# Kernel optimization log

Measured on AMD Instinct MI355X. Metric: run time of the kernel, lower is better.

The kernel has to match this reference:

```python
import jax, jax.numpy as jnp
import numpy as np

N = 50000
E = 1600000
IN_DIM = 32
EDGE_DIM = 32
HID = 64
OUT = 32


def setup_inputs() -> dict:
    key = jax.random.key(0)
    ks = jax.random.split(key, 12)
    x = jax.random.normal(ks[0], (N, IN_DIM), dtype=jnp.float32)
    edge_index = jax.random.randint(ks[1], (2, E), 0, N, dtype=jnp.int64)
    edge_attr = jax.random.normal(ks[2], (E, EDGE_DIM), dtype=jnp.float32)
    # MLP params: Linear(64->64), Linear(64->128), Linear(128->64), Linear(64->32)
    def lin(k, fan_in, fan_out):
        lim = 1.0 / np.sqrt(fan_in)
        kw, kb = jax.random.split(k)
        W = jax.random.uniform(kw, (fan_in, fan_out), minval=-lim, maxval=lim, dtype=jnp.float32)
        b = jax.random.uniform(kb, (fan_out,), minval=-lim, maxval=lim, dtype=jnp.float32)
        return W, b
    W1, b1 = lin(ks[3], IN_DIM + EDGE_DIM, HID)
    W2, b2 = lin(ks[4], HID, 2 * HID)
    W3, b3 = lin(ks[5], 2 * HID, HID)
    W4, b4 = lin(ks[6], HID, OUT)
    return {"x": x, "edge_index": edge_index, "edge_attr": edge_attr,
            "W1": W1, "b1": b1, "W2": W2, "b2": b2,
            "W3": W3, "b3": b3, "W4": W4, "b4": b4}


def reference(x, edge_index, edge_attr, W1, b1, W2, b2, W3, b3, W4, b4):
    # PyG MessagePassing (source_to_target): x_i = x[edge_index[1]] (target),
    # messages aggregated (mean) at target nodes edge_index[1].
    dst = edge_index[1]
    x_i = x[dst]                                   # [E, IN_DIM] gather
    m = jnp.concatenate([x_i, edge_attr], axis=-1)  # [E, 64]
    # 4-layer MLP with ReLU (dropout = identity at inference)
    m = jax.nn.relu(m @ W1 + b1)                   # [E, 64]
    m = jax.nn.relu(m @ W2 + b2)                   # [E, 128]
    m = jax.nn.relu(m @ W3 + b3)                   # [E, 64]
    m = jax.nn.relu(m @ W4 + b4)                   # [E, 32]
    # mean scatter to target nodes
    sums = jax.ops.segment_sum(m, dst, num_segments=N)          # [N, 32]
    cnt = jax.ops.segment_sum(jnp.ones((E,), m.dtype), dst, num_segments=N)
    out = sums / jnp.maximum(cnt, 1.0)[:, None]
    return out
```

## Files before the change

kernel.cpp:

```cpp
#include <hip/hip_runtime.h>
#include <hip/hip_bf16.h>

typedef __attribute__((ext_vector_type(8))) unsigned short u16x8;
typedef __attribute__((ext_vector_type(8))) __bf16 bf16x8;
typedef __attribute__((ext_vector_type(4))) float f32x4;

__device__ __forceinline__ unsigned pack_bf2(float lo, float hi) {
  unsigned a = __float_as_uint(lo) + 0x8000u;
  unsigned b = __float_as_uint(hi) + 0x8000u;
  return __builtin_amdgcn_perm(b, a, 0x07060302);
}

__device__ __forceinline__ unsigned short f2bf(float f) {
  unsigned u = __float_as_uint(f);
  return (unsigned short)((u + 0x7fffu + ((u >> 16) & 1u)) >> 16);
}

__device__ __forceinline__ int aswz(int row, int feat, int stride) {
  return row * stride + (((feat >> 3) ^ (row & 7)) << 4) + (feat & 7) * 2;
}

__global__ void prep_weights(const float* __restrict__ W1, const float* __restrict__ W2,
                             const float* __restrict__ W3, const float* __restrict__ W4,
                             unsigned short* __restrict__ wt) {
  int i = blockIdx.x * 256 + threadIdx.x;
  if (i >= 22528) return;
  float v; int n, k, K, base;
  if (i < 4096)       { n = i >> 6, k = i & 63;  K = 64;  base = 0;     v = W1[k * 64 + n]; }
  else if (i < 12288) { int j = i - 4096;  n = j >> 6, k = j & 63;  K = 64;  base = 4096;  v = W2[k * 128 + n]; }
  else if (i < 20480) { int j = i - 12288; n = j >> 7, k = j & 127; K = 128; base = 12288; v = W3[k * 64 + n]; }
  else                { int j = i - 20480; n = j >> 6, k = j & 63;  K = 64;  base = 20480; v = W4[k * 32 + n]; }
  int o = base + n * K + ((((k >> 3) ^ (n & 7)) << 3) + (k & 7));
  wt[o] = f2bf(v);
}

__global__ void hist_kernel(const int* __restrict__ ei, int* __restrict__ histI, int E) {
  int e = blockIdx.x * 256 + threadIdx.x;
  if (e < E) atomicAdd(&histI[ei[E + e]], 1);
}

__global__ void scan_blocks(const int* __restrict__ histI, int* __restrict__ row_start,
                            int* __restrict__ blockSums, int N) {
  __shared__ int wsum[4];
  const int lane = threadIdx.x & 63, w = threadIdx.x >> 6;
  const int i0 = blockIdx.x * 2048 + threadIdx.x * 8;
  int v[8];
#pragma unroll
  for (int j = 0; j < 8; ++j) { int i = i0 + j; v[j] = (i < N) ? histI[i] : 0; }
  int s = 0;
#pragma unroll
  for (int j = 0; j < 8; ++j) { int t = v[j]; v[j] = s; s += t; }
  int ss = s;
#pragma unroll
  for (int d = 1; d < 64; d <<= 1) { int t = __shfl_up(ss, d, 64); if (lane >= d) ss += t; }
  if (lane == 63) wsum[w] = ss;
  __syncthreads();
  int wOff = 0;
#pragma unroll
  for (int k = 0; k < 4; ++k) if (k < w) wOff += wsum[k];
  const int tOff = wOff + (ss - s);
#pragma unroll
  for (int j = 0; j < 8; ++j) { int i = i0 + j; if (i < N) row_start[i] = tOff + v[j]; }
  if (threadIdx.x == 255) blockSums[blockIdx.x] = wOff + ss;
}

__global__ void scan_tops(int* __restrict__ blockSums, int nb) {
  const int lane = threadIdx.x;
  int v = (lane < nb) ? blockSums[lane] : 0;
  int s = v;
#pragma unroll
  for (int d = 1; d < 64; d <<= 1) { int t = __shfl_up(s, d, 64); if (lane >= d) s += t; }
  if (lane < nb) blockSums[lane] = s - v;
}

__global__ void scan_add(int* __restrict__ row_start, const int* __restrict__ blockSums, int N) {
  int i = blockIdx.x * 256 + threadIdx.x;
  if (i < N) row_start[i] += blockSums[i >> 11];
}

__global__ void fill_kernel(const int* __restrict__ ei, const int* __restrict__ row_start,
                            int* __restrict__ wcnt, int2* __restrict__ edlist, int E) {
  int e = blockIdx.x * 256 + threadIdx.x;
  if (e >= E) return;
  int d = ei[E + e];
  int slot = atomicAdd(&wcnt[d], 1);
  edlist[row_start[d] + slot] = make_int2(e, d);
}

template <int MT, int KS, int SS, int DS>
__device__ __forceinline__ void mlp_layer(const unsigned char* src, unsigned char* dst,
                                          const unsigned char* wl, const float* biasL, int lane) {
  const int edge = lane & 15, g = lane >> 4;
  asm volatile("s_waitcnt lgkmcnt(0)" ::: "memory");
  u16x8 bfrag[KS];
#pragma unroll
  for (int ks = 0; ks < KS; ++ks)
    bfrag[ks] = *(const u16x8*)(src + aswz(edge, ks * 32 + g * 8, SS));
#pragma unroll
  for (int mt = 0; mt < MT; ++mt) {
    const int n = mt * 16 + edge;
    u16x8 af[KS];
#pragma unroll
    for (int ks = 0; ks < KS; ++ks)
      af[ks] = *(const u16x8*)(wl + n * (KS * 64) + (((ks * 4 + g) ^ (edge & 7)) << 4));
    const float4 bv = *(const float4*)(biasL + mt * 16 + g * 4);
    f32x4 acc = {bv.x, bv.y, bv.z, bv.w};
    __builtin_amdgcn_s_setprio(1);
#pragma unroll
    for (int ks = 0; ks < KS; ++ks)
      acc = __builtin_amdgcn_mfma_f32_16x16x32_bf16(
          __builtin_bit_cast(bf16x8, af[ks]), __builtin_bit_cast(bf16x8, bfrag[ks]),
          acc, 0, 0, 0);
    __builtin_amdgcn_s_setprio(0);
    const int fb = mt * 16 + g * 4;
    uint2 q;
    q.x = pack_bf2(fmaxf(acc[0], 0.f), fmaxf(acc[1], 0.f));
    q.y = pack_bf2(fmaxf(acc[2], 0.f), fmaxf(acc[3], 0.f));
    *(uint2*)(dst + aswz(edge, fb, DS)) = q;
  }
}

__device__ __forceinline__ void load_tile(int ebase, int E, const int2* __restrict__ edlist,
                                          const float* __restrict__ x, const float* __restrict__ ea,
                                          int lane, float4& xa, float4& xb, float4& ya, float4& yb,
                                          int& dstA) {
  const int el = ebase + (lane >> 2);
  const int part = lane & 3;
  xa = make_float4(0.f, 0.f, 0.f, 0.f); xb = xa; ya = xa; yb = xa;
  if (el < E) {
    const int2 ed = edlist[el];
    const float4* xp = (const float4*)(x + (size_t)ed.y * 32 + part * 8);
    xa = xp[0]; xb = xp[1];
    const float4* ep = (const float4*)(ea + (size_t)ed.x * 32 + part * 8);
    ya = ep[0]; yb = ep[1];
  }
  const int pos = ebase + (lane & 15);
  dstA = (pos < E) ? edlist[pos].y : -1;
}

#define BIAS_OFF   45056
#define ACT_OFF    46208

__global__ __launch_bounds__(1024, 4)
void gnn_main(const float* __restrict__ x, const int2* __restrict__ edlist,
              const float* __restrict__ ea, const unsigned short* __restrict__ wt,
              const float* __restrict__ b1, const float* __restrict__ b2,
              const float* __restrict__ b3, const float* __restrict__ b4,
              float* __restrict__ out, int E, int numTiles) {
  __shared__ __align__(16) unsigned char lds[ACT_OFF + 16 * 6144];
  {
    const u16x8* gw = (const u16x8*)wt;
    u16x8* lw = (u16x8*)lds;
    for (int i = threadIdx.x; i < 2816; i += 1024) lw[i] = gw[i];
    float* biasW = (float*)(lds + BIAS_OFF);
    for (int i = threadIdx.x; i < 288; i += 1024) {
      float v;
      if (i < 64) v = b1[i];
      else if (i < 192) v = b2[i - 64];
      else if (i < 256) v = b3[i - 192];
      else v = b4[i - 256];
      biasW[i] = v;
    }
  }
  __syncthreads();

  const int lane = threadIdx.x & 63, wid = threadIdx.x >> 6;
  const int edge = lane & 15, g = lane >> 4;
  const float* biasLds = (const float*)(lds + BIAS_OFF);
  unsigned char* buf0 = lds + ACT_OFF + wid * 6144;
  unsigned char* buf1 = buf0 + 4096;
  const unsigned char* wl1 = lds;
  const unsigned char* wl2 = lds + 8192;
  const unsigned char* wl3 = lds + 24576;
  const unsigned char* wl4 = lds + 40960;

  const int wgl = blockIdx.x * 16 + wid;
  const int wstride = gridDim.x * 16;

  float4 xa, xb, ya, yb; int dstA = -1;
  if (wgl < numTiles) load_tile(wgl * 16, E, edlist, x, ea, lane, xa, xb, ya, yb, dstA);

  for (int tile = wgl; tile < numTiles; tile += wstride) {
    uint4 hx, he;
    hx.x = pack_bf2(xa.x, xa.y); hx.y = pack_bf2(xa.z, xa.w);
    hx.z = pack_bf2(xb.x, xb.y); hx.w = pack_bf2(xb.z, xb.w);
    he.x = pack_bf2(ya.x, ya.y); he.y = pack_bf2(ya.z, ya.w);
    he.z = pack_bf2(yb.x, yb.y); he.w = pack_bf2(yb.z, yb.w);
    const int e2 = lane >> 2, part = lane & 3;
    *(uint4*)(buf0 + aswz(e2, part * 8, 256)) = hx;
    *(uint4*)(buf0 + aswz(e2, 32 + part * 8, 256)) = he;

    const int curDst = dstA;

    const int nt = tile + wstride;
    float4 nxa, nxb, nya, nyb; int ndst = -1;
    if (nt < numTiles) load_tile(nt * 16, E, edlist, x, ea, lane, nxa, nxb, nya, nyb, ndst);
    else { nxa = make_float4(0,0,0,0); nxb = nxa; nya = nxa; nyb = nxa; }

    mlp_layer<4, 2, 256, 128>(buf0, buf1, wl1, biasLds + 0,   lane);
    mlp_layer<8, 2, 128, 256>(buf1, buf0, wl2, biasLds + 64,  lane);
    mlp_layer<4, 4, 256, 128>(buf0, buf1, wl3, biasLds + 192, lane);

    asm volatile("s_waitcnt lgkmcnt(0)" ::: "memory");
    u16x8 bf4[2];
#pragma unroll
    for (int ks = 0; ks < 2; ++ks)
      bf4[ks] = *(const u16x8*)(buf1 + aswz(edge, ks * 32 + g * 8, 128));
    float vals[8];
#pragma unroll
    for (int mt = 0; mt < 2; ++mt) {
      const int n = mt * 16 + edge;
      u16x8 af[2];
#pragma unroll
      for (int ks = 0; ks < 2; ++ks)
        af[ks] = *(const u16x8*)(wl4 + n * 128 + (((ks * 4 + g) ^ (edge & 7)) << 4));
      const float4 bv = *(const float4*)(biasLds + 256 + mt * 16 + g * 4);
      f32x4 acc = {bv.x, bv.y, bv.z, bv.w};
      __builtin_amdgcn_s_setprio(1);
#pragma unroll
      for (int ks = 0; ks < 2; ++ks)
        acc = __builtin_amdgcn_mfma_f32_16x16x32_bf16(
            __builtin_bit_cast(bf16x8, af[ks]), __builtin_bit_cast(bf16x8, bf4[ks]),
            acc, 0, 0, 0);
      __builtin_amdgcn_s_setprio(0);
#pragma unroll
      for (int r = 0; r < 4; ++r) vals[mt * 4 + r] = fmaxf(acc[r], 0.f);
    }

    const int li = edge;
    const int prev = __shfl_up(curDst, 1, 16);
    const bool is_head = (li == 0) || (prev != curDst);
    const unsigned long long hb = __ballot(is_head);
    const unsigned gm = (unsigned)((hb >> (g * 16)) & 0xFFFFu);
    const unsigned below = gm & ((1u << li) | ((1u << li) - 1u));
    const int dist = li - (31 - __clz(below));
#pragma unroll
    for (int d = 1; d < 16; d <<= 1) {
#pragma unroll
      for (int t = 0; t < 8; ++t) {
        const float tv = __shfl_up(vals[t], d, 16);
        if (dist >= d) vals[t] += tv;
      }
    }
    const bool is_end = (li == 15) || ((gm >> (li + 1)) & 1u);
    if (is_end && curDst >= 0) {
      float* op = out + (size_t)curDst * 32 + g * 4;
#pragma unroll
      for (int t = 0; t < 4; ++t) unsafeAtomicAdd(op + t, vals[t]);
#pragma unroll
      for (int t = 0; t < 4; ++t) unsafeAtomicAdd(op + 16 + t, vals[4 + t]);
    }

    xa = nxa; xb = nxb; ya = nya; yb = nyb; dstA = ndst;
  }
}

__global__ void div_kernel(float* __restrict__ out, const int* __restrict__ histI, int total) {
  int i = blockIdx.x * 256 + threadIdx.x;
  if (i < total) out[i] = out[i] / fmaxf((float)histI[i >> 5], 1.0f);
}

extern "C" void kernel_launch(void* const* d_in, const int* in_sizes, int n_in,
                              void* d_out, int out_size, void* d_ws, size_t ws_size,
                              hipStream_t stream) {
  const float* x  = (const float*)d_in[0];
  const int*   ei = (const int*)d_in[1];
  const float* ea = (const float*)d_in[2];
  const float* W1 = (const float*)d_in[3];
  const float* b1 = (const float*)d_in[4];
  const float* W2 = (const float*)d_in[5];
  const float* b2 = (const float*)d_in[6];
  const float* W3 = (const float*)d_in[7];
  const float* b3 = (const float*)d_in[8];
  const float* W4 = (const float*)d_in[9];
  const float* b4 = (const float*)d_in[10];
  const int N = in_sizes[0] / 32;
  const int E = in_sizes[1] / 2;
  float* out = (float*)d_out;

  char* ws = (char*)d_ws;
  size_t off = 0;
  auto alloc = [&](size_t bytes) { size_t o = off; off += (bytes + 255) & ~(size_t)255; return o; };
  int* histI      = (int*)(ws + alloc((size_t)N * 4));
  int* wcnt       = (int*)(ws + alloc((size_t)N * 4));
  int* row_start  = (int*)(ws + alloc((size_t)(N + 1) * 4));
  int* blockSums  = (int*)(ws + alloc(64 * 4));
  int2* edlist    = (int2*)(ws + alloc((size_t)E * 8));
  unsigned short* wt = (unsigned short*)(ws + alloc(22528 * 2));

  hipMemsetAsync(d_out, 0, (size_t)out_size * sizeof(float), stream);
  hipMemsetAsync(histI, 0, (size_t)N * 4, stream);
  hipMemsetAsync(wcnt, 0, (size_t)N * 4, stream);

  prep_weights<<<(22528 + 255) / 256, 256, 0, stream>>>(W1, W2, W3, W4, wt);
  hist_kernel<<<(E + 255) / 256, 256, 0, stream>>>(ei, histI, E);
  const int nb = (N + 2047) / 2048;
  scan_blocks<<<nb, 256, 0, stream>>>(histI, row_start, blockSums, N);
  scan_tops<<<1, 64, 0, stream>>>(blockSums, nb);
  scan_add<<<(N + 255) / 256, 256, 0, stream>>>(row_start, blockSums, N);
  fill_kernel<<<(E + 255) / 256, 256, 0, stream>>>(ei, row_start, wcnt, edlist, E);

  const int numTiles = (E + 15) / 16;
  gnn_main<<<256, 1024, 0, stream>>>(x, edlist, ea, wt, b1, b2, b3, b4, out, E, numTiles);
  const int total = N * 32;
  div_kernel<<<(total + 255) / 256, 256, 0, stream>>>(out, histI, total);
}
```

Measured before the change: 334.1 us.

## Process 32-edge tiles per wave and fuse prep, scan-add and memset kernels

The main kernel now handles 32 edges per wave instead of 16, so each weight A-fragment loaded from LDS feeds two MFMA sub-tiles. It moves to 512-thread blocks with 8 waves and doubles the per-wave LDS activation buffers. On the host side, weight prep is fused with the histogram, scan_add is folded into fill_kernel, output zeroing moves into fill_kernel, and two memsets become one. Together these cut launch count and LDS weight traffic, at the cost of more registers per wave and fewer resident waves per block.

```diff
diff --git a/kernel.cpp b/kernel.cpp
--- a/kernel.cpp
+++ b/kernel.cpp
@@ -20,23 +20,21 @@
   return row * stride + (((feat >> 3) ^ (row & 7)) << 4) + (feat & 7) * 2;
 }
 
-__global__ void prep_weights(const float* __restrict__ W1, const float* __restrict__ W2,
-                             const float* __restrict__ W3, const float* __restrict__ W4,
-                             unsigned short* __restrict__ wt) {
+__global__ void prep_hist(const float* __restrict__ W1, const float* __restrict__ W2,
+                          const float* __restrict__ W3, const float* __restrict__ W4,
+                          unsigned short* __restrict__ wt,
+                          const int* __restrict__ ei, int* __restrict__ histI, int E) {
   int i = blockIdx.x * 256 + threadIdx.x;
-  if (i >= 22528) return;
-  float v; int n, k, K, base;
-  if (i < 4096)       { n = i >> 6, k = i & 63;  K = 64;  base = 0;     v = W1[k * 64 + n]; }
-  else if (i < 12288) { int j = i - 4096;  n = j >> 6, k = j & 63;  K = 64;  base = 4096;  v = W2[k * 128 + n]; }
-  else if (i < 20480) { int j = i - 12288; n = j >> 7, k = j & 127; K = 128; base = 12288; v = W3[k * 64 + n]; }
-  else                { int j = i - 20480; n = j >> 6, k = j & 63;  K = 64;  base = 20480; v = W4[k * 32 + n]; }
-  int o = base + n * K + ((((k >> 3) ^ (n & 7)) << 3) + (k & 7));
-  wt[o] = f2bf(v);
-}
-
-__global__ void hist_kernel(const int* __restrict__ ei, int* __restrict__ histI, int E) {
-  int e = blockIdx.x * 256 + threadIdx.x;
-  if (e < E) atomicAdd(&histI[ei[E + e]], 1);
+  if (i < 22528) {
+    float v; int n, k, K, base;
+    if (i < 4096)       { n = i >> 6, k = i & 63;  K = 64;  base = 0;     v = W1[k * 64 + n]; }
+    else if (i < 12288) { int j = i - 4096;  n = j >> 6, k = j & 63;  K = 64;  base = 4096;  v = W2[k * 128 + n]; }
+    else if (i < 20480) { int j = i - 12288; n = j >> 7, k = j & 127; K = 128; base = 12288; v = W3[k * 64 + n]; }
+    else                { int j = i - 20480; n = j >> 6, k = j & 63;  K = 64;  base = 20480; v = W4[k * 32 + n]; }
+    int o = base + n * K + ((((k >> 3) ^ (n & 7)) << 3) + (k & 7));
+    wt[o] = f2bf(v);
+  }
+  if (i < E) atomicAdd(&histI[ei[E + i]], 1);
 }
 
 __global__ void scan_blocks(const int* __restrict__ histI, int* __restrict__ row_start,
@@ -73,29 +71,29 @@
   if (lane < nb) blockSums[lane] = s - v;
 }
 
-__global__ void scan_add(int* __restrict__ row_start, const int* __restrict__ blockSums, int N) {
-  int i = blockIdx.x * 256 + threadIdx.x;
-  if (i < N) row_start[i] += blockSums[i >> 11];
-}
-
 __global__ void fill_kernel(const int* __restrict__ ei, const int* __restrict__ row_start,
-                            int* __restrict__ wcnt, int2* __restrict__ edlist, int E) {
+                            const int* __restrict__ blockSums, int* __restrict__ wcnt,
+                            int2* __restrict__ edlist, float* __restrict__ out,
+                            int E, int Ntot) {
   int e = blockIdx.x * 256 + threadIdx.x;
+  if (e < Ntot) out[e] = 0.0f;
   if (e >= E) return;
   int d = ei[E + e];
   int slot = atomicAdd(&wcnt[d], 1);
-  edlist[row_start[d] + slot] = make_int2(e, d);
+  edlist[row_start[d] + blockSums[d >> 11] + slot] = make_int2(e, d);
 }
 
 template <int MT, int KS, int SS, int DS>
-__device__ __forceinline__ void mlp_layer(const unsigned char* src, unsigned char* dst,
-                                          const unsigned char* wl, const float* biasL, int lane) {
+__device__ __forceinline__ void mlp_layer2(const unsigned char* src, unsigned char* dst,
+                                           const unsigned char* wl, const float* biasL, int lane) {
   const int edge = lane & 15, g = lane >> 4;
   asm volatile("s_waitcnt lgkmcnt(0)" ::: "memory");
-  u16x8 bfrag[KS];
-#pragma unroll
-  for (int ks = 0; ks < KS; ++ks)
-    bfrag[ks] = *(const u16x8*)(src + aswz(edge, ks * 32 + g * 8, SS));
+  u16x8 bfrag[2][KS];
+#pragma unroll
+  for (int s = 0; s < 2; ++s)
+#pragma unroll
+    for (int ks = 0; ks < KS; ++ks)
+      bfrag[s][ks] = *(const u16x8*)(src + aswz(s * 16 + edge, ks * 32 + g * 8, SS));
 #pragma unroll
   for (int mt = 0; mt < MT; ++mt) {
     const int n = mt * 16 + edge;
@@ -104,56 +102,61 @@
     for (int ks = 0; ks < KS; ++ks)
       af[ks] = *(const u16x8*)(wl + n * (KS * 64) + (((ks * 4 + g) ^ (edge & 7)) << 4));
     const float4 bv = *(const float4*)(biasL + mt * 16 + g * 4);
-    f32x4 acc = {bv.x, bv.y, bv.z, bv.w};
-    __builtin_amdgcn_s_setprio(1);
-#pragma unroll
-    for (int ks = 0; ks < KS; ++ks)
-      acc = __builtin_amdgcn_mfma_f32_16x16x32_bf16(
-          __builtin_bit_cast(bf16x8, af[ks]), __builtin_bit_cast(bf16x8, bfrag[ks]),
-          acc, 0, 0, 0);
-    __builtin_amdgcn_s_setprio(0);
-    const int fb = mt * 16 + g * 4;
-    uint2 q;
-    q.x = pack_bf2(fmaxf(acc[0], 0.f), fmaxf(acc[1], 0.f));
-    q.y = pack_bf2(fmaxf(acc[2], 0.f), fmaxf(acc[3], 0.f));
-    *(uint2*)(dst + aswz(edge, fb, DS)) = q;
-  }
-}
-
-__device__ __forceinline__ void load_tile(int ebase, int E, const int2* __restrict__ edlist,
-                                          const float* __restrict__ x, const float* __restrict__ ea,
-                                          int lane, float4& xa, float4& xb, float4& ya, float4& yb,
-                                          int& dstA) {
-  const int el = ebase + (lane >> 2);
-  const int part = lane & 3;
-  xa = make_float4(0.f, 0.f, 0.f, 0.f); xb = xa; ya = xa; yb = xa;
+#pragma unroll
+    for (int s = 0; s < 2; ++s) {
+      f32x4 acc = {bv.x, bv.y, bv.z, bv.w};
+      __builtin_amdgcn_s_setprio(1);
+#pragma unroll
+      for (int ks = 0; ks < KS; ++ks)
+        acc = __builtin_amdgcn_mfma_f32_16x16x32_bf16(
+            __builtin_bit_cast(bf16x8, af[ks]), __builtin_bit_cast(bf16x8, bfrag[s][ks]),
+            acc, 0, 0, 0);
+      __builtin_amdgcn_s_setprio(0);
+      const int fb = mt * 16 + g * 4;
+      uint2 q;
+      q.x = pack_bf2(fmaxf(acc[0], 0.f), fmaxf(acc[1], 0.f));
+      q.y = pack_bf2(fmaxf(acc[2], 0.f), fmaxf(acc[3], 0.f));
+      *(uint2*)(dst + aswz(s * 16 + edge, fb, DS)) = q;
+    }
+  }
+}
+
+__device__ __forceinline__ void load_tile32(int ebase, int E, const int2* __restrict__ edlist,
+                                            const float* __restrict__ x, const float* __restrict__ ea,
+                                            int lane, float4 (&px)[4], float4 (&pe)[4],
+                                            int& d0, int& d1) {
+  const int el = ebase + (lane >> 1);
+  const int part = lane & 1;
+#pragma unroll
+  for (int j = 0; j < 4; ++j) { px[j] = make_float4(0.f, 0.f, 0.f, 0.f); pe[j] = px[j]; }
   if (el < E) {
     const int2 ed = edlist[el];
-    const float4* xp = (const float4*)(x + (size_t)ed.y * 32 + part * 8);
-    xa = xp[0]; xb = xp[1];
-    const float4* ep = (const float4*)(ea + (size_t)ed.x * 32 + part * 8);
-    ya = ep[0]; yb = ep[1];
-  }
-  const int pos = ebase + (lane & 15);
-  dstA = (pos < E) ? edlist[pos].y : -1;
-}
-
-#define BIAS_OFF   45056
-#define ACT_OFF    46208
-
-__global__ __launch_bounds__(1024, 4)
+    const float4* xp = (const float4*)(x + (size_t)ed.y * 32 + part * 16);
+    const float4* ep = (const float4*)(ea + (size_t)ed.x * 32 + part * 16);
+#pragma unroll
+    for (int j = 0; j < 4; ++j) { px[j] = xp[j]; pe[j] = ep[j]; }
+  }
+  const int p0 = ebase + (lane & 15), p1 = p0 + 16;
+  d0 = (p0 < E) ? edlist[p0].y : -1;
+  d1 = (p1 < E) ? edlist[p1].y : -1;
+}
+
+#define BIAS_OFF 45056
+#define ACT_OFF  46208
+
+__global__ __launch_bounds__(512, 2)
 void gnn_main(const float* __restrict__ x, const int2* __restrict__ edlist,
               const float* __restrict__ ea, const unsigned short* __restrict__ wt,
               const float* __restrict__ b1, const float* __restrict__ b2,
               const float* __restrict__ b3, const float* __restrict__ b4,
               float* __restrict__ out, int E, int numTiles) {
-  __shared__ __align__(16) unsigned char lds[ACT_OFF + 16 * 6144];
+  __shared__ __align__(16) unsigned char lds[ACT_OFF + 8 * 12288];
   {
     const u16x8* gw = (const u16x8*)wt;
     u16x8* lw = (u16x8*)lds;
-    for (int i = threadIdx.x; i < 2816; i += 1024) lw[i] = gw[i];
+    for (int i = threadIdx.x; i < 2816; i += 512) lw[i] = gw[i];
     float* biasW = (float*)(lds + BIAS_OFF);
-    for (int i = threadIdx.x; i < 288; i += 1024) {
+    for (int i = threadIdx.x; i < 288; i += 512) {
       float v;
       if (i < 64) v = b1[i];
       else if (i < 192) v = b2[i - 64];
@@ -167,91 +170,110 @@
   const int lane = threadIdx.x & 63, wid = threadIdx.x >> 6;
   const int edge = lane & 15, g = lane >> 4;
   const float* biasLds = (const float*)(lds + BIAS_OFF);
-  unsigned char* buf0 = lds + ACT_OFF + wid * 6144;
-  unsigned char* buf1 = buf0 + 4096;
+  unsigned char* X = lds + ACT_OFF + wid * 12288;
+  unsigned char* Y = X + 8192;
   const unsigned char* wl1 = lds;
   const unsigned char* wl2 = lds + 8192;
   const unsigned char* wl3 = lds + 24576;
   const unsigned char* wl4 = lds + 40960;
 
-  const int wgl = blockIdx.x * 16 + wid;
-  const int wstride = gridDim.x * 16;
-
-  float4 xa, xb, ya, yb; int dstA = -1;
-  if (wgl < numTiles) load_tile(wgl * 16, E, edlist, x, ea, lane, xa, xb, ya, yb, dstA);
+  const int wgl = blockIdx.x * 8 + wid;
+  const int wstride = gridDim.x * 8;
+
+  float4 px[4], pe[4]; int d0 = -1, d1 = -1;
+  if (wgl < numTiles) load_tile32(wgl * 32, E, edlist, x, ea, lane, px, pe, d0, d1);
 
   for (int tile = wgl; tile < numTiles; tile += wstride) {
-    uint4 hx, he;
-    hx.x = pack_bf2(xa.x, xa.y); hx.y = pack_bf2(xa.z, xa.w);
-    hx.z = pack_bf2(xb.x, xb.y); hx.w = pack_bf2(xb.z, xb.w);
-    he.x = pack_bf2(ya.x, ya.y); he.y = pack_bf2(ya.z, ya.w);
-    he.z = pack_bf2(yb.x, yb.y); he.w = pack_bf2(yb.z, yb.w);
-    const int e2 = lane >> 2, part = lane & 3;
-    *(uint4*)(buf0 + aswz(e2, part * 8, 256)) = hx;
-    *(uint4*)(buf0 + aswz(e2, 32 + part * 8, 256)) = he;
-
-    const int curDst = dstA;
+    const int row = lane >> 1, part = lane & 1;
+    {
+      uint4 qa, qb;
+      qa.x = pack_bf2(px[0].x, px[0].y); qa.y = pack_bf2(px[0].z, px[0].w);
+      qa.z = pack_bf2(px[1].x, px[1].y); qa.w = pack_bf2(px[1].z, px[1].w);
+      qb.x = pack_bf2(px[2].x, px[2].y); qb.y = pack_bf2(px[2].z, px[2].w);
+      qb.z = pack_bf2(px[3].x, px[3].y); qb.w = pack_bf2(px[3].z, px[3].w);
+      *(uint4*)(X + aswz(row, part * 16, 256)) = qa;
+      *(uint4*)(X + aswz(row, part * 16 + 8, 256)) = qb;
+      qa.x = pack_bf2(pe[0].x, pe[0].y); qa.y = pack_bf2(pe[0].z, pe[0].w);
+      qa.z = pack_bf2(pe[1].x, pe[1].y); qa.w = pack_bf2(pe[1].z, pe[1].w);
+      qb.x = pack_bf2(pe[2].x, pe[2].y); qb.y = pack_bf2(pe[2].z, pe[2].w);
+      qb.z = pack_bf2(pe[3].x, pe[3].y); qb.w = pack_bf2(pe[3].z, pe[3].w);
+      *(uint4*)(X + aswz(row, 32 + part * 16, 256)) = qa;
+      *(uint4*)(X + aswz(row, 32 + part * 16 + 8, 256)) = qb;
+    }
+    const int cd0 = d0, cd1 = d1;
 
     const int nt = tile + wstride;
-    float4 nxa, nxb, nya, nyb; int ndst = -1;
-    if (nt < numTiles) load_tile(nt * 16, E, edlist, x, ea, lane, nxa, nxb, nya, nyb, ndst);
-    else { nxa = make_float4(0,0,0,0); nxb = nxa; nya = nxa; nyb = nxa; }
-
-    mlp_layer<4, 2, 256, 128>(buf0, buf1, wl1, biasLds + 0,   lane);
-    mlp_layer<8, 2, 128, 256>(buf1, buf0, wl2, biasLds + 64,  lane);
-    mlp_layer<4, 4, 256, 128>(buf0, buf1, wl3, biasLds + 192, lane);
+    float4 npx[4], npe[4]; int nd0 = -1, nd1 = -1;
+    if (nt < numTiles) load_tile32(nt * 32, E, edlist, x, ea, lane, npx, npe, nd0, nd1);
+    else {
+#pragma unroll
+      for (int j = 0; j < 4; ++j) { npx[j] = make_float4(0.f,0.f,0.f,0.f); npe[j] = npx[j]; }
+    }
+
+    mlp_layer2<4, 2, 256, 128>(X, Y, wl1, biasLds + 0,   lane);
+    mlp_layer2<8, 2, 128, 256>(Y, X, wl2, biasLds + 64,  lane);
+    mlp_layer2<4, 4, 256, 128>(X, Y, wl3, biasLds + 192, lane);
 
     asm volatile("s_waitcnt lgkmcnt(0)" ::: "memory");
-    u16x8 bf4[2];
-#pragma unroll
-    for (int ks = 0; ks < 2; ++ks)
-      bf4[ks] = *(const u16x8*)(buf1 + aswz(edge, ks * 32 + g * 8, 128));
-    float vals[8];
-#pragma unroll
-    for (int mt = 0; mt < 2; ++mt) {
-      const int n = mt * 16 + edge;
-      u16x8 af[2];
+    u16x8 bf4[2][2];
+#pragma unroll
+    for (int s = 0; s < 2; ++s)
 #pragma unroll
       for (int ks = 0; ks < 2; ++ks)
-        af[ks] = *(const u16x8*)(wl4 + n * 128 + (((ks * 4 + g) ^ (edge & 7)) << 4));
-      const float4 bv = *(const float4*)(biasLds + 256 + mt * 16 + g * 4);
-      f32x4 acc = {bv.x, bv.y, bv.z, bv.w};
-      __builtin_amdgcn_s_setprio(1);
+        bf4[s][ks] = *(const u16x8*)(Y + aswz(s * 16 + edge, ks * 32 + g * 8, 128));
+    u16x8 af4[2][2];
+#pragma unroll
+    for (int mt = 0; mt < 2; ++mt)
 #pragma unroll
       for (int ks = 0; ks < 2; ++ks)
-        acc = __builtin_amdgcn_mfma_f32_16x16x32_bf16(
-            __builtin_bit_cast(bf16x8, af[ks]), __builtin_bit_cast(bf16x8, bf4[ks]),
-            acc, 0, 0, 0);
-      __builtin_amdgcn_s_setprio(0);
-#pragma unroll
-      for (int r = 0; r < 4; ++r) vals[mt * 4 + r] = fmaxf(acc[r], 0.f);
-    }
-
-    const int li = edge;
-    const int prev = __shfl_up(curDst, 1, 16);
-    const bool is_head = (li == 0) || (prev != curDst);
-    const unsigned long long hb = __ballot(is_head);
-    const unsigned gm = (unsigned)((hb >> (g * 16)) & 0xFFFFu);
-    const unsigned below = gm & ((1u << li) | ((1u << li) - 1u));
-    const int dist = li - (31 - __clz(below));
-#pragma unroll
-    for (int d = 1; d < 16; d <<= 1) {
-#pragma unroll
-      for (int t = 0; t < 8; ++t) {
-        const float tv = __shfl_up(vals[t], d, 16);
-        if (dist >= d) vals[t] += tv;
+        af4[mt][ks] = *(const u16x8*)(wl4 + (mt * 16 + edge) * 128 + (((ks * 4 + g) ^ (edge & 7)) << 4));
+
+#pragma unroll
+    for (int s = 0; s < 2; ++s) {
+      float vals[8];
+#pragma unroll
+      for (int mt = 0; mt < 2; ++mt) {
+        const float4 bv = *(const float4*)(biasLds + 256 + mt * 16 + g * 4);
+        f32x4 acc = {bv.x, bv.y, bv.z, bv.w};
+        __builtin_amdgcn_s_setprio(1);
+#pragma unroll
+        for (int ks = 0; ks < 2; ++ks)
+          acc = __builtin_amdgcn_mfma_f32_16x16x32_bf16(
+              __builtin_bit_cast(bf16x8, af4[mt][ks]), __builtin_bit_cast(bf16x8, bf4[s][ks]),
+              acc, 0, 0, 0);
+        __builtin_amdgcn_s_setprio(0);
+#pragma unroll
+        for (int r = 0; r < 4; ++r) vals[mt * 4 + r] = fmaxf(acc[r], 0.f);
       }
-    }
-    const bool is_end = (li == 15) || ((gm >> (li + 1)) & 1u);
-    if (is_end && curDst >= 0) {
-      float* op = out + (size_t)curDst * 32 + g * 4;
-#pragma unroll
-      for (int t = 0; t < 4; ++t) unsafeAtomicAdd(op + t, vals[t]);
-#pragma unroll
-      for (int t = 0; t < 4; ++t) unsafeAtomicAdd(op + 16 + t, vals[4 + t]);
-    }
-
-    xa = nxa; xb = nxb; ya = nya; yb = nyb; dstA = ndst;
+      const int curDst = s ? cd1 : cd0;
+      const int li = edge;
+      const int prev = __shfl_up(curDst, 1, 16);
+      const bool is_head = (li == 0) || (prev != curDst);
+      const unsigned long long hb = __ballot(is_head);
+      const unsigned gm = (unsigned)((hb >> (g * 16)) & 0xFFFFu);
+      const unsigned below = gm & ((1u << li) | ((1u << li) - 1u));
+      const int dist = li - (31 - __clz(below));
+#pragma unroll
+      for (int d = 1; d < 16; d <<= 1) {
+#pragma unroll
+        for (int t = 0; t < 8; ++t) {
+          const float tv = __shfl_up(vals[t], d, 16);
+          if (dist >= d) vals[t] += tv;
+        }
+      }
+      const bool is_end = (li == 15) || ((gm >> (li + 1)) & 1u);
+      if (is_end && curDst >= 0) {
+        float* op = out + (size_t)curDst * 32 + g * 4;
+#pragma unroll
+        for (int t = 0; t < 4; ++t) unsafeAtomicAdd(op + t, vals[t]);
+#pragma unroll
+        for (int t = 0; t < 4; ++t) unsafeAtomicAdd(op + 16 + t, vals[4 + t]);
+      }
+    }
+
+#pragma unroll
+    for (int j = 0; j < 4; ++j) { px[j] = npx[j]; pe[j] = npe[j]; }
+    d0 = nd0; d1 = nd1;
   }
 }
 
@@ -281,27 +303,27 @@
   char* ws = (char*)d_ws;
   size_t off = 0;
   auto alloc = [&](size_t bytes) { size_t o = off; off += (bytes + 255) & ~(size_t)255; return o; };
-  int* histI      = (int*)(ws + alloc((size_t)N * 4));
-  int* wcnt       = (int*)(ws + alloc((size_t)N * 4));
+  size_t hist_off = alloc((size_t)N * 4);
+  size_t wcnt_off = alloc((size_t)N * 4);
+  int* histI      = (int*)(ws + hist_off);
+  int* wcnt       = (int*)(ws + wcnt_off);
   int* row_start  = (int*)(ws + alloc((size_t)(N + 1) * 4));
   int* blockSums  = (int*)(ws + alloc(64 * 4));
   int2* edlist    = (int2*)(ws + alloc((size_t)E * 8));
   unsigned short* wt = (unsigned short*)(ws + alloc(22528 * 2));
 
-  hipMemsetAsync(d_out, 0, (size_t)out_size * sizeof(float), stream);
-  hipMemsetAsync(histI, 0, (size_t)N * 4, stream);
-  hipMemsetAsync(wcnt, 0, (size_t)N * 4, stream);
-
-  prep_weights<<<(22528 + 255) / 256, 256, 0, stream>>>(W1, W2, W3, W4, wt);
-  hist_kernel<<<(E + 255) / 256, 256, 0, stream>>>(ei, histI, E);
+  hipMemsetAsync(ws + hist_off, 0, (wcnt_off - hist_off) + (size_t)N * 4, stream);
+
+  const int gridPH = (max(E, 22528) + 255) / 256;
+  prep_hist<<<gridPH, 256, 0, stream>>>(W1, W2, W3, W4, wt, ei, histI, E);
   const int nb = (N + 2047) / 2048;
   scan_blocks<<<nb, 256, 0, stream>>>(histI, row_start, blockSums, N);
   scan_tops<<<1, 64, 0, stream>>>(blockSums, nb);
-  scan_add<<<(N + 255) / 256, 256, 0, stream>>>(row_start, blockSums, N);
-  fill_kernel<<<(E + 255) / 256, 256, 0, stream>>>(ei, row_start, wcnt, edlist, E);
-
-  const int numTiles = (E + 15) / 16;
-  gnn_main<<<256, 1024, 0, stream>>>(x, edlist, ea, wt, b1, b2, b3, b4, out, E, numTiles);
-  const int total = N * 32;
-  div_kernel<<<(total + 255) / 256, 256, 0, stream>>>(out, histI, total);
-}
+  const int Ntot = N * 32;
+  const int gridF = (max(E, Ntot) + 255) / 256;
+  fill_kernel<<<gridF, 256, 0, stream>>>(ei, row_start, blockSums, wcnt, edlist, out, E, Ntot);
+
+  const int numTiles = (E + 31) / 32;
+  gnn_main<<<256, 512, 0, stream>>>(x, edlist, ea, wt, b1, b2, b3, b4, out, E, numTiles);
+  div_kernel<<<(Ntot + 255) / 256, 256, 0, stream>>>(out, histI, Ntot);
+}
```

After: 349.9 us. 1.05x slower.

## Fuse preprocessing kernels, keep MLP weights in registers, fold mean division into atomics

Applied to the files above, without the earlier changes.

Merges the weight-prep and histogram kernels, and folds the scan top-level and scan-add steps into the fill kernel, which also zeroes the output. The separate divide kernel is removed by scaling each segment sum by 1/count before the atomic add. The main kernel now holds all MLP weight fragments in registers instead of reading them from LDS, with smaller 256-thread blocks and a different grid. The aim is fewer launches and less LDS traffic per layer, at the cost of heavy register pressure that may lower occupancy, and it vectorises edge-index reads in the atomics kernels.

```diff
diff --git a/kernel.cpp b/kernel.cpp
--- a/kernel.cpp
+++ b/kernel.cpp
@@ -20,23 +20,28 @@
   return row * stride + (((feat >> 3) ^ (row & 7)) << 4) + (feat & 7) * 2;
 }
 
-__global__ void prep_weights(const float* __restrict__ W1, const float* __restrict__ W2,
-                             const float* __restrict__ W3, const float* __restrict__ W4,
-                             unsigned short* __restrict__ wt) {
+__global__ void prep_hist(const float* __restrict__ W1, const float* __restrict__ W2,
+                          const float* __restrict__ W3, const float* __restrict__ W4,
+                          unsigned short* __restrict__ wt,
+                          const int* __restrict__ ei, int* __restrict__ histI, int E) {
   int i = blockIdx.x * 256 + threadIdx.x;
-  if (i >= 22528) return;
-  float v; int n, k, K, base;
-  if (i < 4096)       { n = i >> 6, k = i & 63;  K = 64;  base = 0;     v = W1[k * 64 + n]; }
-  else if (i < 12288) { int j = i - 4096;  n = j >> 6, k = j & 63;  K = 64;  base = 4096;  v = W2[k * 128 + n]; }
-  else if (i < 20480) { int j = i - 12288; n = j >> 7, k = j & 127; K = 128; base = 12288; v = W3[k * 64 + n]; }
-  else                { int j = i - 20480; n = j >> 6, k = j & 63;  K = 64;  base = 20480; v = W4[k * 32 + n]; }
-  int o = base + n * K + ((((k >> 3) ^ (n & 7)) << 3) + (k & 7));
-  wt[o] = f2bf(v);
-}
-
-__global__ void hist_kernel(const int* __restrict__ ei, int* __restrict__ histI, int E) {
-  int e = blockIdx.x * 256 + threadIdx.x;
-  if (e < E) atomicAdd(&histI[ei[E + e]], 1);
+  if (i < 22528) {
+    float v; int n, k, K, base;
+    if (i < 4096)       { n = i >> 6, k = i & 63;  K = 64;  base = 0;     v = W1[k * 64 + n]; }
+    else if (i < 12288) { int j = i - 4096;  n = j >> 6, k = j & 63;  K = 64;  base = 4096;  v = W2[k * 128 + n]; }
+    else if (i < 20480) { int j = i - 12288; n = j >> 7, k = j & 127; K = 128; base = 12288; v = W3[k * 64 + n]; }
+    else                { int j = i - 20480; n = j >> 6, k = j & 63;  K = 64;  base = 20480; v = W4[k * 32 + n]; }
+    int o = base + n * K + ((((k >> 3) ^ (n & 7)) << 3) + (k & 7));
+    wt[o] = f2bf(v);
+  }
+  const int e0 = i * 4;
+  if (e0 + 3 < E) {
+    const int4 d4 = *(const int4*)(ei + E + e0);
+    atomicAdd(&histI[d4.x], 1); atomicAdd(&histI[d4.y], 1);
+    atomicAdd(&histI[d4.z], 1); atomicAdd(&histI[d4.w], 1);
+  } else {
+    for (int e = e0; e < E; ++e) atomicAdd(&histI[ei[E + e]], 1);
+  }
 }
 
 __global__ void scan_blocks(const int* __restrict__ histI, int* __restrict__ row_start,
@@ -64,32 +69,41 @@
   if (threadIdx.x == 255) blockSums[blockIdx.x] = wOff + ss;
 }
 
-__global__ void scan_tops(int* __restrict__ blockSums, int nb) {
-  const int lane = threadIdx.x;
-  int v = (lane < nb) ? blockSums[lane] : 0;
-  int s = v;
-#pragma unroll
-  for (int d = 1; d < 64; d <<= 1) { int t = __shfl_up(s, d, 64); if (lane >= d) s += t; }
-  if (lane < nb) blockSums[lane] = s - v;
-}
-
-__global__ void scan_add(int* __restrict__ row_start, const int* __restrict__ blockSums, int N) {
-  int i = blockIdx.x * 256 + threadIdx.x;
-  if (i < N) row_start[i] += blockSums[i >> 11];
-}
-
 __global__ void fill_kernel(const int* __restrict__ ei, const int* __restrict__ row_start,
-                            int* __restrict__ wcnt, int2* __restrict__ edlist, int E) {
-  int e = blockIdx.x * 256 + threadIdx.x;
-  if (e >= E) return;
-  int d = ei[E + e];
-  int slot = atomicAdd(&wcnt[d], 1);
-  edlist[row_start[d] + slot] = make_int2(e, d);
+                            const int* __restrict__ blockSums, int* __restrict__ wcnt,
+                            int2* __restrict__ edlist, float* __restrict__ out,
+                            int E, int Ntot4, int nb) {
+  __shared__ int spre[64];
+  if (threadIdx.x == 0) {
+    int acc = 0;
+    for (int k = 0; k < nb; ++k) { spre[k] = acc; acc += blockSums[k]; }
+  }
+  __syncthreads();
+  const int t = blockIdx.x * 256 + threadIdx.x;
+  if (t < Ntot4) *(float4*)(out + t * 4) = make_float4(0.f, 0.f, 0.f, 0.f);
+  const int e0 = t * 4;
+  if (e0 + 3 < E) {
+    const int4 d4 = *(const int4*)(ei + E + e0);
+    const int dv[4] = {d4.x, d4.y, d4.z, d4.w};
+#pragma unroll
+    for (int j = 0; j < 4; ++j) {
+      const int d = dv[j];
+      const int slot = atomicAdd(&wcnt[d], 1);
+      edlist[row_start[d] + spre[d >> 11] + slot] = make_int2(e0 + j, d);
+    }
+  } else {
+    for (int e = e0; e < E; ++e) {
+      const int d = ei[E + e];
+      const int slot = atomicAdd(&wcnt[d], 1);
+      edlist[row_start[d] + spre[d >> 11] + slot] = make_int2(e, d);
+    }
+  }
 }
 
 template <int MT, int KS, int SS, int DS>
-__device__ __forceinline__ void mlp_layer(const unsigned char* src, unsigned char* dst,
-                                          const unsigned char* wl, const float* biasL, int lane) {
+__device__ __forceinline__ void mlp_layerR(const unsigned char* src, unsigned char* dst,
+                                           const u16x8 (&wf)[MT][KS],
+                                           const float* biasL, int lane) {
   const int edge = lane & 15, g = lane >> 4;
   asm volatile("s_waitcnt lgkmcnt(0)" ::: "memory");
   u16x8 bfrag[KS];
@@ -98,18 +112,13 @@
     bfrag[ks] = *(const u16x8*)(src + aswz(edge, ks * 32 + g * 8, SS));
 #pragma unroll
   for (int mt = 0; mt < MT; ++mt) {
-    const int n = mt * 16 + edge;
-    u16x8 af[KS];
-#pragma unroll
-    for (int ks = 0; ks < KS; ++ks)
-      af[ks] = *(const u16x8*)(wl + n * (KS * 64) + (((ks * 4 + g) ^ (edge & 7)) << 4));
     const float4 bv = *(const float4*)(biasL + mt * 16 + g * 4);
     f32x4 acc = {bv.x, bv.y, bv.z, bv.w};
     __builtin_amdgcn_s_setprio(1);
 #pragma unroll
     for (int ks = 0; ks < KS; ++ks)
       acc = __builtin_amdgcn_mfma_f32_16x16x32_bf16(
-          __builtin_bit_cast(bf16x8, af[ks]), __builtin_bit_cast(bf16x8, bfrag[ks]),
+          __builtin_bit_cast(bf16x8, wf[mt][ks]), __builtin_bit_cast(bf16x8, bfrag[ks]),
           acc, 0, 0, 0);
     __builtin_amdgcn_s_setprio(0);
     const int fb = mt * 16 + g * 4;
@@ -122,8 +131,9 @@
 
 __device__ __forceinline__ void load_tile(int ebase, int E, const int2* __restrict__ edlist,
                                           const float* __restrict__ x, const float* __restrict__ ea,
+                                          const int* __restrict__ histI,
                                           int lane, float4& xa, float4& xb, float4& ya, float4& yb,
-                                          int& dstA) {
+                                          int& dstA, int& cntA) {
   const int el = ebase + (lane >> 2);
   const int part = lane & 3;
   xa = make_float4(0.f, 0.f, 0.f, 0.f); xb = xa; ya = xa; yb = xa;
@@ -135,50 +145,69 @@
     ya = ep[0]; yb = ep[1];
   }
   const int pos = ebase + (lane & 15);
-  dstA = (pos < E) ? edlist[pos].y : -1;
-}
-
-#define BIAS_OFF   45056
-#define ACT_OFF    46208
-
-__global__ __launch_bounds__(1024, 4)
+  dstA = -1; cntA = 1;
+  if (pos < E) {
+    dstA = edlist[pos].y;
+    cntA = histI[dstA];
+  }
+}
+
+__global__ __launch_bounds__(256, 2)
 void gnn_main(const float* __restrict__ x, const int2* __restrict__ edlist,
               const float* __restrict__ ea, const unsigned short* __restrict__ wt,
+              const int* __restrict__ histI,
               const float* __restrict__ b1, const float* __restrict__ b2,
               const float* __restrict__ b3, const float* __restrict__ b4,
               float* __restrict__ out, int E, int numTiles) {
-  __shared__ __align__(16) unsigned char lds[ACT_OFF + 16 * 6144];
-  {
-    const u16x8* gw = (const u16x8*)wt;
-    u16x8* lw = (u16x8*)lds;
-    for (int i = threadIdx.x; i < 2816; i += 1024) lw[i] = gw[i];
-    float* biasW = (float*)(lds + BIAS_OFF);
-    for (int i = threadIdx.x; i < 288; i += 1024) {
-      float v;
-      if (i < 64) v = b1[i];
-      else if (i < 192) v = b2[i - 64];
-      else if (i < 256) v = b3[i - 192];
-      else v = b4[i - 256];
-      biasW[i] = v;
-    }
+  __shared__ __align__(16) unsigned char lds[1152 + 4 * 6144];
+  float* biasW = (float*)lds;
+  for (int i = threadIdx.x; i < 288; i += 256) {
+    float v;
+    if (i < 64) v = b1[i];
+    else if (i < 192) v = b2[i - 64];
+    else if (i < 256) v = b3[i - 192];
+    else v = b4[i - 256];
+    biasW[i] = v;
   }
   __syncthreads();
 
   const int lane = threadIdx.x & 63, wid = threadIdx.x >> 6;
   const int edge = lane & 15, g = lane >> 4;
-  const float* biasLds = (const float*)(lds + BIAS_OFF);
-  unsigned char* buf0 = lds + ACT_OFF + wid * 6144;
+  const float* biasLds = (const float*)lds;
+  unsigned char* buf0 = lds + 1152 + wid * 6144;
   unsigned char* buf1 = buf0 + 4096;
-  const unsigned char* wl1 = lds;
-  const unsigned char* wl2 = lds + 8192;
-  const unsigned char* wl3 = lds + 24576;
-  const unsigned char* wl4 = lds + 40960;
-
-  const int wgl = blockIdx.x * 16 + wid;
-  const int wstride = gridDim.x * 16;
-
-  float4 xa, xb, ya, yb; int dstA = -1;
-  if (wgl < numTiles) load_tile(wgl * 16, E, edlist, x, ea, lane, xa, xb, ya, yb, dstA);
+
+  const unsigned short* w1t = wt;
+  const unsigned short* w2t = wt + 4096;
+  const unsigned short* w3t = wt + 12288;
+  const unsigned short* w4t = wt + 20480;
+  u16x8 wf1[4][2], wf2[8][2], wf3[4][4], wf4[2][2];
+#pragma unroll
+  for (int mt = 0; mt < 4; ++mt)
+#pragma unroll
+    for (int ks = 0; ks < 2; ++ks)
+      wf1[mt][ks] = *(const u16x8*)(w1t + (mt * 16 + edge) * 64 + (((ks * 4 + g) ^ (edge & 7)) << 3));
+#pragma unroll
+  for (int mt = 0; mt < 8; ++mt)
+#pragma unroll
+    for (int ks = 0; ks < 2; ++ks)
+      wf2[mt][ks] = *(const u16x8*)(w2t + (mt * 16 + edge) * 64 + (((ks * 4 + g) ^ (edge & 7)) << 3));
+#pragma unroll
+  for (int mt = 0; mt < 4; ++mt)
+#pragma unroll
+    for (int ks = 0; ks < 4; ++ks)
+      wf3[mt][ks] = *(const u16x8*)(w3t + (mt * 16 + edge) * 128 + (((ks * 4 + g) ^ (edge & 7)) << 3));
+#pragma unroll
+  for (int mt = 0; mt < 2; ++mt)
+#pragma unroll
+    for (int ks = 0; ks < 2; ++ks)
+      wf4[mt][ks] = *(const u16x8*)(w4t + (mt * 16 + edge) * 64 + (((ks * 4 + g) ^ (edge & 7)) << 3));
+
+  const int wgl = blockIdx.x * 4 + wid;
+  const int wstride = gridDim.x * 4;
+
+  float4 xa, xb, ya, yb; int dstA = -1, cntA = 1;
+  if (wgl < numTiles) load_tile(wgl * 16, E, edlist, x, ea, histI, lane, xa, xb, ya, yb, dstA, cntA);
 
   for (int tile = wgl; tile < numTiles; tile += wstride) {
     uint4 hx, he;
@@ -190,16 +219,16 @@
     *(uint4*)(buf0 + aswz(e2, part * 8, 256)) = hx;
     *(uint4*)(buf0 + aswz(e2, 32 + part * 8, 256)) = he;
 
-    const int curDst = dstA;
+    const int curDst = dstA, curCnt = cntA;
 
     const int nt = tile + wstride;
-    float4 nxa, nxb, nya, nyb; int ndst = -1;
-    if (nt < numTiles) load_tile(nt * 16, E, edlist, x, ea, lane, nxa, nxb, nya, nyb, ndst);
+    float4 nxa, nxb, nya, nyb; int nd = -1, nc = 1;
+    if (nt < numTiles) load_tile(nt * 16, E, edlist, x, ea, histI, lane, nxa, nxb, nya, nyb, nd, nc);
     else { nxa = make_float4(0,0,0,0); nxb = nxa; nya = nxa; nyb = nxa; }
 
-    mlp_layer<4, 2, 256, 128>(buf0, buf1, wl1, biasLds + 0,   lane);
-    mlp_layer<8, 2, 128, 256>(buf1, buf0, wl2, biasLds + 64,  lane);
-    mlp_layer<4, 4, 256, 128>(buf0, buf1, wl3, biasLds + 192, lane);
+    mlp_layerR<4, 2, 256, 128>(buf0, buf1, wf1, biasLds + 0,   lane);
+    mlp_layerR<8, 2, 128, 256>(buf1, buf0, wf2, biasLds + 64,  lane);
+    mlp_layerR<4, 4, 256, 128>(buf0, buf1, wf3, biasLds + 192, lane);
 
     asm volatile("s_waitcnt lgkmcnt(0)" ::: "memory");
     u16x8 bf4[2];
@@ -209,18 +238,13 @@
     float vals[8];
 #pragma unroll
     for (int mt = 0; mt < 2; ++mt) {
-      const int n = mt * 16 + edge;
-      u16x8 af[2];
-#pragma unroll
-      for (int ks = 0; ks < 2; ++ks)
-        af[ks] = *(const u16x8*)(wl4 + n * 128 + (((ks * 4 + g) ^ (edge & 7)) << 4));
       const float4 bv = *(const float4*)(biasLds + 256 + mt * 16 + g * 4);
       f32x4 acc = {bv.x, bv.y, bv.z, bv.w};
       __builtin_amdgcn_s_setprio(1);
 #pragma unroll
       for (int ks = 0; ks < 2; ++ks)
         acc = __builtin_amdgcn_mfma_f32_16x16x32_bf16(
-            __builtin_bit_cast(bf16x8, af[ks]), __builtin_bit_cast(bf16x8, bf4[ks]),
+            __builtin_bit_cast(bf16x8, wf4[mt][ks]), __builtin_bit_cast(bf16x8, bf4[ks]),
             acc, 0, 0, 0);
       __builtin_amdgcn_s_setprio(0);
 #pragma unroll
@@ -244,20 +268,16 @@
     }
     const bool is_end = (li == 15) || ((gm >> (li + 1)) & 1u);
     if (is_end && curDst >= 0) {
+      const float inv = 1.0f / (float)curCnt;
       float* op = out + (size_t)curDst * 32 + g * 4;
 #pragma unroll
-      for (int t = 0; t < 4; ++t) unsafeAtomicAdd(op + t, vals[t]);
-#pragma unroll
-      for (int t = 0; t < 4; ++t) unsafeAtomicAdd(op + 16 + t, vals[4 + t]);
-    }
-
-    xa = nxa; xb = nxb; ya = nya; yb = nyb; dstA = ndst;
-  }
-}
-
-__global__ void div_kernel(float* __restrict__ out, const int* __restrict__ histI, int total) {
-  int i = blockIdx.x * 256 + threadIdx.x;
-  if (i < total) out[i] = out[i] / fmaxf((float)histI[i >> 5], 1.0f);
+      for (int t = 0; t < 4; ++t) unsafeAtomicAdd(op + t, vals[t] * inv);
+#pragma unroll
+      for (int t = 0; t < 4; ++t) unsafeAtomicAdd(op + 16 + t, vals[4 + t] * inv);
+    }
+
+    xa = nxa; xb = nxb; ya = nya; yb = nyb; dstA = nd; cntA = nc;
+  }
 }
 
 extern "C" void kernel_launch(void* const* d_in, const int* in_sizes, int n_in,
@@ -281,27 +301,26 @@
   char* ws = (char*)d_ws;
   size_t off = 0;
   auto alloc = [&](size_t bytes) { size_t o = off; off += (bytes + 255) & ~(size_t)255; return o; };
-  int* histI      = (int*)(ws + alloc((size_t)N * 4));
-  int* wcnt       = (int*)(ws + alloc((size_t)N * 4));
+  size_t hist_off = alloc((size_t)N * 4);
+  size_t wcnt_off = alloc((size_t)N * 4);
+  int* histI      = (int*)(ws + hist_off);
+  int* wcnt       = (int*)(ws + wcnt_off);
   int* row_start  = (int*)(ws + alloc((size_t)(N + 1) * 4));
   int* blockSums  = (int*)(ws + alloc(64 * 4));
   int2* edlist    = (int2*)(ws + alloc((size_t)E * 8));
   unsigned short* wt = (unsigned short*)(ws + alloc(22528 * 2));
 
-  hipMemsetAsync(d_out, 0, (size_t)out_size * sizeof(float), stream);
-  hipMemsetAsync(histI, 0, (size_t)N * 4, stream);
-  hipMemsetAsync(wcnt, 0, (size_t)N * 4, stream);
-
-  prep_weights<<<(22528 + 255) / 256, 256, 0, stream>>>(W1, W2, W3, W4, wt);
-  hist_kernel<<<(E + 255) / 256, 256, 0, stream>>>(ei, histI, E);
+  hipMemsetAsync(ws + hist_off, 0, (wcnt_off - hist_off) + (size_t)N * 4, stream);
+
+  const int quarters = (E + 3) / 4;
+  const int gridPH = (max(quarters, 22528) + 255) / 256;
+  prep_hist<<<gridPH, 256, 0, stream>>>(W1, W2, W3, W4, wt, ei, histI, E);
   const int nb = (N + 2047) / 2048;
   scan_blocks<<<nb, 256, 0, stream>>>(histI, row_start, blockSums, N);
-  scan_tops<<<1, 64, 0, stream>>>(blockSums, nb);
-  scan_add<<<(N + 255) / 256, 256, 0, stream>>>(row_start, blockSums, N);
-  fill_kernel<<<(E + 255) / 256, 256, 0, stream>>>(ei, row_start, wcnt, edlist, E);
+  const int Ntot4 = (N * 32) / 4;
+  const int gridF = (max(quarters, Ntot4) + 255) / 256;
+  fill_kernel<<<gridF, 256, 0, stream>>>(ei, row_start, blockSums, wcnt, edlist, out, E, Ntot4, nb);
 
   const int numTiles = (E + 15) / 16;
-  gnn_main<<<256, 1024, 0, stream>>>(x, edlist, ea, wt, b1, b2, b3, b4, out, E, numTiles);
-  const int total = N * 32;
-  div_kernel<<<(total + 255) / 256, 256, 0, stream>>>(out, histI, total);
-}
+  gnn_main<<<512, 256, 0, stream>>>(x, edlist, ea, wt, histI, b1, b2, b3, b4, out, E, numTiles);
+}
```

Measured after the change: 376.6 us. +12.7%, slower.
